# Performance work log

Measured on AMD Instinct MI355X. Metric: run time of the kernel, lower is better.

Reference implementation:

```python
import jax, jax.numpy as jnp
import numpy as np

TEMPERATURE = 0.5
EPS = 1e-8  # F.cosine_similarity eps


def _neg_mask_indices(B):
    # mask: ones, zero diagonal, zero the two positive off-diagonals
    N = 2 * B
    mask = np.ones((N, N), dtype=bool)
    np.fill_diagonal(mask, False)
    idx = np.arange(B)
    mask[idx, idx + B] = False
    mask[idx + B, idx] = False
    rows, cols = np.nonzero(mask)  # static, computed at trace time
    return rows, cols


def setup_inputs() -> dict:
    key = jax.random.key(0)
    k1, k2 = jax.random.split(key)
    B, D = 4096, 128
    z_i = jax.random.normal(k1, (B, D), dtype=jnp.float32)
    z_j = jax.random.normal(k2, (B, D), dtype=jnp.float32)
    return {"z_i": z_i, "z_j": z_j}


def reference(z_i, z_j):
    B = z_i.shape[0]
    N = 2 * B
    z = jnp.concatenate([z_i, z_j], axis=0)  # [N, D]
    norm = jnp.maximum(jnp.linalg.norm(z, axis=1, keepdims=True), EPS)
    zn = z / norm
    sim = (zn @ zn.T) / TEMPERATURE  # [N, N] cosine similarity / temp

    # positives: the i <-> i+B pairs
    sim_i_j = jnp.diagonal(sim, offset=B)
    sim_j_i = jnp.diagonal(sim, offset=-B)
    positives = jnp.concatenate([sim_i_j, sim_j_i], axis=0)[:, None]  # [N, 1]

    rows, cols = _neg_mask_indices(B)
    negatives = sim[rows, cols].reshape(N, N - 2)  # [N, N-2]

    logits = jnp.concatenate([positives, negatives], axis=1)  # [N, N-1]
    # cross-entropy with labels == 0 (positive is column 0)
    loss = jnp.mean(jax.nn.logsumexp(logits, axis=1) - logits[:, 0])
    return loss
```

## Files before the change

kernel.cpp:

```cpp
#include <hip/hip_runtime.h>
#include <hip/hip_bf16.h>
#include <math.h>


typedef __attribute__((ext_vector_type(8))) short bf16x8;
typedef __attribute__((ext_vector_type(4))) float f32x4;

#define NROWS 8192
#define DDIM  128
#define BHALF 4096
#define CHUNK 32
#define TILE  128
#define NT    64
#define NBLK  2080
#define CPAD  136
#define SQRT_E2S 1.6986435980707531f
#define TWO_LN2  1.3862943611198906f
#define EXPDIAG  7.38905609893065f

static __device__ __forceinline__ unsigned short f2bf(float f) {
  unsigned int u = __float_as_uint(f);
  unsigned int r = (u + 0x7fffu + ((u >> 16) & 1u)) >> 16;
  return (unsigned short)r;
}

static __device__ __forceinline__ void glds16(const unsigned short* g, unsigned short* l) {
  __builtin_amdgcn_global_load_lds((const __attribute__((address_space(1))) unsigned int*)g,
                                   (__attribute__((address_space(3))) unsigned int*)l,
                                   16, 0, 0);
}

__global__ void norm_kernel(const float* __restrict__ zi, const float* __restrict__ zj,
                            unsigned short* __restrict__ zn,
                            float* __restrict__ pos, float* __restrict__ out) {
  __shared__ float2 xbuf[2][64];
  int wave = threadIdx.x >> 6;
  int lane = threadIdx.x & 63;
  int pi   = blockIdx.x * 2 + (wave & 1);
  int row  = pi + (wave >> 1) * BHALF;
  const float* src = (row < BHALF) ? (zi + (size_t)row * DDIM)
                                   : (zj + (size_t)(row - BHALF) * DDIM);
  float2 v = *(const float2*)(src + 2 * lane);
  float ss = v.x * v.x + v.y * v.y;
  #pragma unroll
  for (int off = 1; off < 64; off <<= 1) ss += __shfl_xor(ss, off);
  float scale = SQRT_E2S / fmaxf(sqrtf(ss), 1e-8f);
  v.x *= scale; v.y *= scale;
  unsigned int lo = f2bf(v.x), hi = f2bf(v.y);
  ((unsigned int*)(zn + (size_t)row * DDIM))[lane] = lo | (hi << 16);

  if (wave >= 2) xbuf[wave - 2][lane] = v;
  __syncthreads();
  if (wave < 2) {
    float2 w = xbuf[wave][lane];
    float d = v.x * w.x + v.y * w.y;
    #pragma unroll
    for (int off = 1; off < 64; off <<= 1) d += __shfl_xor(d, off);
    if (lane == 0) pos[pi] = d;
  }
  if (blockIdx.x == 0 && threadIdx.x == 0) out[0] = 0.0f;
}

__global__ __launch_bounds__(256, 2)
void sim_kernel(const unsigned short* __restrict__ zn, float* __restrict__ part) {
  __shared__ unsigned short lds[2 * CHUNK * DDIM];
  __shared__ float colpart[16][CPAD];

  int t = blockIdx.x;
  int tx = (int)((129.0f - sqrtf((float)(16641 - 8 * t))) * 0.5f);
  while ((tx + 1) * NT - ((tx + 1) * tx) / 2 <= t) ++tx;
  while (tx * NT - (tx * (tx - 1)) / 2 > t) --tx;
  const int ty = t - (tx * NT - (tx * (tx - 1)) / 2) + tx;
  const bool diag = (tx == ty);

  const int wave = threadIdx.x >> 6;
  const int lane = threadIdx.x & 63;
  const int l15  = lane & 15;
  const int quad = lane >> 4;

  const int row_base = tx * TILE + wave * 32;
  const int col_base = ty * TILE;

  bf16x8 a[2][4];
  const unsigned short* abase = zn + (size_t)(row_base + l15) * DDIM + quad * 8;
  #pragma unroll
  for (int mi = 0; mi < 2; ++mi)
    #pragma unroll
    for (int kf = 0; kf < 4; ++kf)
      a[mi][kf] = *(const bf16x8*)(abase + mi * 16 * DDIM + kf * 32);

  float rs[2][4];
  #pragma unroll
  for (int mi = 0; mi < 2; ++mi)
    #pragma unroll
    for (int r = 0; r < 4; ++r) rs[mi][r] = 0.0f;

  const int t0 = wave * 64 + lane;
  const int r0 = t0 >> 4,         c0 = (t0 & 15) ^ (r0 & 15);
  const int r1 = (t0 + 256) >> 4, c1 = (t0 & 15) ^ (r1 & 15);
  const unsigned short* gst0 = zn + (size_t)(col_base + r0) * DDIM + c0 * 8;
  const unsigned short* gst1 = zn + (size_t)(col_base + r1) * DDIM + c1 * 8;

  int rdoff[4];
  #pragma unroll
  for (int kf = 0; kf < 4; ++kf)
    rdoff[kf] = l15 * DDIM + (((quad + 4 * kf) ^ l15) << 3);

  float* cp = &colpart[wave * 4 + quad][l15];

  glds16(gst0, lds + wave * 512);
  glds16(gst1, lds + 2048 + wave * 512);
  __syncthreads();

  for (int ch = 0; ch < 4; ++ch) {
    const int buf = ch & 1;
    if (ch < 3) {
      const unsigned short* g0 = gst0 + (size_t)(ch + 1) * CHUNK * DDIM;
      const unsigned short* g1 = gst1 + (size_t)(ch + 1) * CHUNK * DDIM;
      unsigned short* lb = lds + ((ch + 1) & 1) * 4096;
      glds16(g0, lb + wave * 512);
      glds16(g1, lb + 2048 + wave * 512);
    }
    const unsigned short* lb = lds + buf * 4096;
    #pragma unroll
    for (int ni = 0; ni < 2; ++ni) {
      bf16x8 b[4];
      #pragma unroll
      for (int kf = 0; kf < 4; ++kf)
        b[kf] = *(const bf16x8*)(lb + ni * 16 * DDIM + rdoff[kf]);
      f32x4 acc[2];
      #pragma unroll
      for (int mi = 0; mi < 2; ++mi) {
        f32x4 z = {0.0f, 0.0f, 0.0f, 0.0f};
        acc[mi] = __builtin_amdgcn_mfma_f32_16x16x32_bf16(a[mi][0], b[0], z, 0, 0, 0);
      }
      #pragma unroll
      for (int kf = 1; kf < 4; ++kf)
        #pragma unroll
        for (int mi = 0; mi < 2; ++mi)
          acc[mi] = __builtin_amdgcn_mfma_f32_16x16x32_bf16(a[mi][kf], b[kf], acc[mi], 0, 0, 0);
      float cs = 0.0f;
      #pragma unroll
      for (int mi = 0; mi < 2; ++mi)
        #pragma unroll
        for (int r = 0; r < 4; ++r) {
          float e = __builtin_amdgcn_exp2f(acc[mi][r]);
          rs[mi][r] += e;
          cs += e;
        }
      cp[(ch * 2 + ni) * 16] = cs;
    }
    __syncthreads();
  }

  #pragma unroll
  for (int mi = 0; mi < 2; ++mi)
    #pragma unroll
    for (int r = 0; r < 4; ++r) {
      float v = rs[mi][r];
      v += __shfl_xor(v, 1);
      v += __shfl_xor(v, 2);
      v += __shfl_xor(v, 4);
      v += __shfl_xor(v, 8);
      if (l15 == 0)
        part[(size_t)ty * NROWS + row_base + mi * 16 + quad * 4 + r] = v;
    }
  if (!diag && threadIdx.x < TILE) {
    float v = 0.0f;
    #pragma unroll
    for (int s = 0; s < 16; ++s) v += colpart[s][threadIdx.x];
    part[(size_t)tx * NROWS + col_base + threadIdx.x] = v;
  }
}

__global__ void finalize_kernel(const float* __restrict__ part,
                                const float* __restrict__ pos,
                                float* __restrict__ out) {
  __shared__ float red[4];
  int i = blockIdx.x * 256 + threadIdx.x;
  float si = 0.0f, sp = 0.0f;
  #pragma unroll 8
  for (int s = 0; s < NT; ++s) {
    si += part[(size_t)s * NROWS + i];
    sp += part[(size_t)s * NROWS + i + BHALF];
  }
  si -= EXPDIAG;
  sp -= EXPDIAG;
  float v = logf(si) + logf(sp) - TWO_LN2 * pos[i];
  #pragma unroll
  for (int off = 1; off < 64; off <<= 1) v += __shfl_xor(v, off);
  int wave = threadIdx.x >> 6, lane = threadIdx.x & 63;
  if (lane == 0) red[wave] = v;
  __syncthreads();
  if (threadIdx.x == 0)
    atomicAdd(out, (red[0] + red[1] + red[2] + red[3]) * (1.0f / 8192.0f));
}

extern "C" void kernel_launch(void* const* d_in, const int* in_sizes, int n_in,
                              void* d_out, int out_size, void* d_ws, size_t ws_size,
                              hipStream_t stream) {
  const float* zi = (const float*)d_in[0];
  const float* zj = (const float*)d_in[1];
  char* ws = (char*)d_ws;
  unsigned short* zn = (unsigned short*)ws;
  float* part = (float*)(ws + (size_t)NROWS * DDIM * 2);
  float* pos  = (float*)(ws + (size_t)NROWS * DDIM * 2
                            + (size_t)NT * NROWS * 4);
  float* out = (float*)d_out;

  norm_kernel<<<2048, 256, 0, stream>>>(zi, zj, zn, pos, out);
  sim_kernel<<<NBLK, 256, 0, stream>>>(zn, part);
  finalize_kernel<<<16, 256, 0, stream>>>(part, pos, out);
}
```

Before: 86.53 us.

## Prefetch all column chunks upfront with vmcnt waits and split finalize across more blocks

The sim kernel now issues all four column-chunk global-to-LDS loads at the start into a four-deep LDS buffer. It then waits on each chunk with partial vmcnt counts and a barrier, replacing the double-buffered loop that synchronised every iteration, and raises wave priority around the MFMA block. CPAD loses its padding, and an explicit sync is added before the colpart reduction. Finalize now uses one thread per row across twice as many blocks to spread the partial-sum reads. LDS use per block doubles, and the unpadded colpart may cause bank conflicts.

```diff
diff --git a/kernel.cpp b/kernel.cpp
--- a/kernel.cpp
+++ b/kernel.cpp
@@ -13,9 +13,10 @@
 #define TILE  128
 #define NT    64
 #define NBLK  2080
-#define CPAD  136
+#define CPAD  128
 #define SQRT_E2S 1.6986435980707531f
 #define TWO_LN2  1.3862943611198906f
+#define LN2      0.6931471805599453f
 #define EXPDIAG  7.38905609893065f
 
 static __device__ __forceinline__ unsigned short f2bf(float f) {
@@ -63,7 +64,7 @@
 
 __global__ __launch_bounds__(256, 2)
 void sim_kernel(const unsigned short* __restrict__ zn, float* __restrict__ part) {
-  __shared__ unsigned short lds[2 * CHUNK * DDIM];
+  __shared__ unsigned short lds[4 * CHUNK * DDIM];
   __shared__ float colpart[16][CPAD];
 
   int t = blockIdx.x;
@@ -88,70 +89,76 @@
     #pragma unroll
     for (int kf = 0; kf < 4; ++kf)
       a[mi][kf] = *(const bf16x8*)(abase + mi * 16 * DDIM + kf * 32);
-
-  float rs[2][4];
-  #pragma unroll
-  for (int mi = 0; mi < 2; ++mi)
-    #pragma unroll
-    for (int r = 0; r < 4; ++r) rs[mi][r] = 0.0f;
+  __builtin_amdgcn_sched_barrier(0);
 
   const int t0 = wave * 64 + lane;
   const int r0 = t0 >> 4,         c0 = (t0 & 15) ^ (r0 & 15);
   const int r1 = (t0 + 256) >> 4, c1 = (t0 & 15) ^ (r1 & 15);
   const unsigned short* gst0 = zn + (size_t)(col_base + r0) * DDIM + c0 * 8;
   const unsigned short* gst1 = zn + (size_t)(col_base + r1) * DDIM + c1 * 8;
+  #pragma unroll
+  for (int ch = 0; ch < 4; ++ch) {
+    glds16(gst0 + (size_t)ch * CHUNK * DDIM, lds + ch * 4096 + wave * 512);
+    glds16(gst1 + (size_t)ch * CHUNK * DDIM, lds + ch * 4096 + 2048 + wave * 512);
+  }
+  __builtin_amdgcn_sched_barrier(0);
 
   int rdoff[4];
   #pragma unroll
   for (int kf = 0; kf < 4; ++kf)
     rdoff[kf] = l15 * DDIM + (((quad + 4 * kf) ^ l15) << 3);
 
+  float rs[2][4];
+  #pragma unroll
+  for (int mi = 0; mi < 2; ++mi)
+    #pragma unroll
+    for (int r = 0; r < 4; ++r) rs[mi][r] = 0.0f;
+
   float* cp = &colpart[wave * 4 + quad][l15];
 
-  glds16(gst0, lds + wave * 512);
-  glds16(gst1, lds + 2048 + wave * 512);
-  __syncthreads();
-
-  for (int ch = 0; ch < 4; ++ch) {
-    const int buf = ch & 1;
-    if (ch < 3) {
-      const unsigned short* g0 = gst0 + (size_t)(ch + 1) * CHUNK * DDIM;
-      const unsigned short* g1 = gst1 + (size_t)(ch + 1) * CHUNK * DDIM;
-      unsigned short* lb = lds + ((ch + 1) & 1) * 4096;
-      glds16(g0, lb + wave * 512);
-      glds16(g1, lb + 2048 + wave * 512);
-    }
-    const unsigned short* lb = lds + buf * 4096;
-    #pragma unroll
-    for (int ni = 0; ni < 2; ++ni) {
-      bf16x8 b[4];
-      #pragma unroll
-      for (int kf = 0; kf < 4; ++kf)
-        b[kf] = *(const bf16x8*)(lb + ni * 16 * DDIM + rdoff[kf]);
-      f32x4 acc[2];
-      #pragma unroll
-      for (int mi = 0; mi < 2; ++mi) {
-        f32x4 z = {0.0f, 0.0f, 0.0f, 0.0f};
-        acc[mi] = __builtin_amdgcn_mfma_f32_16x16x32_bf16(a[mi][0], b[0], z, 0, 0, 0);
-      }
-      #pragma unroll
-      for (int kf = 1; kf < 4; ++kf)
-        #pragma unroll
-        for (int mi = 0; mi < 2; ++mi)
-          acc[mi] = __builtin_amdgcn_mfma_f32_16x16x32_bf16(a[mi][kf], b[kf], acc[mi], 0, 0, 0);
-      float cs = 0.0f;
-      #pragma unroll
-      for (int mi = 0; mi < 2; ++mi)
-        #pragma unroll
-        for (int r = 0; r < 4; ++r) {
-          float e = __builtin_amdgcn_exp2f(acc[mi][r]);
-          rs[mi][r] += e;
-          cs += e;
-        }
-      cp[(ch * 2 + ni) * 16] = cs;
-    }
-    __syncthreads();
-  }
+#define SIM_PHASE(CH, VM)                                                      \
+  {                                                                            \
+    asm volatile("s_waitcnt vmcnt(" VM ")" ::: "memory");                      \
+    __builtin_amdgcn_s_barrier();                                              \
+    __builtin_amdgcn_sched_barrier(0);                                         \
+    const unsigned short* lb = lds + (CH) * 4096;                              \
+    _Pragma("unroll")                                                          \
+    for (int ni = 0; ni < 2; ++ni) {                                           \
+      bf16x8 b[4];                                                             \
+      _Pragma("unroll")                                                        \
+      for (int kf = 0; kf < 4; ++kf)                                           \
+        b[kf] = *(const bf16x8*)(lb + ni * 16 * DDIM + rdoff[kf]);             \
+      f32x4 acc[2];                                                            \
+      __builtin_amdgcn_s_setprio(1);                                           \
+      _Pragma("unroll")                                                        \
+      for (int mi = 0; mi < 2; ++mi) {                                         \
+        f32x4 z = {0.0f, 0.0f, 0.0f, 0.0f};                                    \
+        acc[mi] = __builtin_amdgcn_mfma_f32_16x16x32_bf16(a[mi][0], b[0], z, 0, 0, 0); \
+      }                                                                        \
+      _Pragma("unroll")                                                        \
+      for (int kf = 1; kf < 4; ++kf)                                           \
+        _Pragma("unroll")                                                      \
+        for (int mi = 0; mi < 2; ++mi)                                         \
+          acc[mi] = __builtin_amdgcn_mfma_f32_16x16x32_bf16(a[mi][kf], b[kf], acc[mi], 0, 0, 0); \
+      __builtin_amdgcn_s_setprio(0);                                           \
+      float cs = 0.0f;                                                         \
+      _Pragma("unroll")                                                        \
+      for (int mi = 0; mi < 2; ++mi)                                           \
+        _Pragma("unroll")                                                      \
+        for (int r = 0; r < 4; ++r) {                                          \
+          float e = __builtin_amdgcn_exp2f(acc[mi][r]);                        \
+          rs[mi][r] += e;                                                      \
+          cs += e;                                                             \
+        }                                                                      \
+      cp[((CH) * 2 + ni) * 16] = cs;                                           \
+    }                                                                          \
+  }
+
+  SIM_PHASE(0, "6")
+  SIM_PHASE(1, "4")
+  SIM_PHASE(2, "2")
+  SIM_PHASE(3, "0")
+#undef SIM_PHASE
 
   #pragma unroll
   for (int mi = 0; mi < 2; ++mi)
@@ -165,6 +172,7 @@
       if (l15 == 0)
         part[(size_t)ty * NROWS + row_base + mi * 16 + quad * 4 + r] = v;
     }
+  __syncthreads();
   if (!diag && threadIdx.x < TILE) {
     float v = 0.0f;
     #pragma unroll
@@ -177,16 +185,11 @@
                                 const float* __restrict__ pos,
                                 float* __restrict__ out) {
   __shared__ float red[4];
-  int i = blockIdx.x * 256 + threadIdx.x;
-  float si = 0.0f, sp = 0.0f;
-  #pragma unroll 8
-  for (int s = 0; s < NT; ++s) {
-    si += part[(size_t)s * NROWS + i];
-    sp += part[(size_t)s * NROWS + i + BHALF];
-  }
-  si -= EXPDIAG;
-  sp -= EXPDIAG;
-  float v = logf(si) + logf(sp) - TWO_LN2 * pos[i];
+  int r = blockIdx.x * 256 + threadIdx.x;
+  float s = 0.0f;
+  #pragma unroll 16
+  for (int k = 0; k < NT; ++k) s += part[(size_t)k * NROWS + r];
+  float v = logf(s - EXPDIAG) - LN2 * pos[r & (BHALF - 1)];
   #pragma unroll
   for (int off = 1; off < 64; off <<= 1) v += __shfl_xor(v, off);
   int wave = threadIdx.x >> 6, lane = threadIdx.x & 63;
@@ -210,5 +213,5 @@
 
   norm_kernel<<<2048, 256, 0, stream>>>(zi, zj, zn, pos, out);
   sim_kernel<<<NBLK, 256, 0, stream>>>(zn, part);
-  finalize_kernel<<<16, 256, 0, stream>>>(part, pos, out);
-}
+  finalize_kernel<<<32, 256, 0, stream>>>(part, pos, out);
+}
```

New measurement: 81.18 us. -6.2%, faster.
